# Optimization experiments

Hardware: AMD Instinct MI355X
Metric: run time of the kernel (lower is better)

Reference implementation:

```python
import jax, jax.numpy as jnp
import numpy as np

F = 256      # n_features
N = 128      # n_nodes
B = 4096     # batch


def setup_inputs() -> dict:
    key = jax.random.key(0)
    ks = jax.random.split(key, 11)
    s = lambda *sh: 1.0 / np.sqrt(sh[-2]) if len(sh) >= 2 else 1.0
    x = jax.random.normal(ks[0], (B, F), dtype=jnp.float32)
    # Block-diagonal weights: [F, in, out] per stage; biases [F, out]
    w1 = jax.random.normal(ks[1], (F, 1, N), dtype=jnp.float32)
    b1 = jax.random.normal(ks[2], (F, N), dtype=jnp.float32) * 0.01
    w2 = jax.random.normal(ks[3], (F, N, N), dtype=jnp.float32) / np.sqrt(N)
    b2 = jax.random.normal(ks[4], (F, N), dtype=jnp.float32) * 0.01
    w3 = jax.random.normal(ks[5], (F, N, N), dtype=jnp.float32) / np.sqrt(N)
    b3 = jax.random.normal(ks[6], (F, N), dtype=jnp.float32) * 0.01
    w4 = jax.random.normal(ks[7], (F, N, 1), dtype=jnp.float32) / np.sqrt(N)
    b4 = jax.random.normal(ks[8], (F, 1), dtype=jnp.float32) * 0.01
    # Final linear: [F, 1] weight, [1] bias
    lr_w = jax.random.normal(ks[9], (F, 1), dtype=jnp.float32) / np.sqrt(F)
    lr_b = jax.random.normal(ks[10], (1,), dtype=jnp.float32) * 0.01
    return {"x": x, "w1": w1, "b1": b1, "w2": w2, "b2": b2,
            "w3": w3, "b3": b3, "w4": w4, "b4": b4,
            "lr_w": lr_w, "lr_b": lr_b}


def reference(x, w1, b1, w2, b2, w3, b3, w4, b4, lr_w, lr_b):
    # Per-feature block-diagonal MLP chain with ReLU between stages.
    # x: [B, F] -> view each feature as a 1-dim input to its own subnet.
    h = x[:, :, None]                                   # [B, F, 1]
    h = jax.nn.relu(jnp.einsum('bfi,fio->bfo', h, w1) + b1)   # [B, F, N]
    h = jax.nn.relu(jnp.einsum('bfi,fio->bfo', h, w2) + b2)   # [B, F, N]
    h = jax.nn.relu(jnp.einsum('bfi,fio->bfo', h, w3) + b3)   # [B, F, N]
    h = jnp.einsum('bfi,fio->bfo', h, w4) + b4                # [B, F, 1]
    x_pre = h[:, :, 0]                                        # [B, F]
    return x_pre @ lr_w + lr_b                                # [B, 1]
```

## Files before the change

### kernel.cpp

```cpp
#include <hip/hip_runtime.h>
#include <hip/hip_bf16.h>

#define F_DIM 256
#define N_DIM 128
#define B_DIM 4096

typedef float f32x4v __attribute__((ext_vector_type(4)));
typedef float f32x16v __attribute__((ext_vector_type(16)));
typedef short s16x8 __attribute__((ext_vector_type(8)));
typedef unsigned int u32x4v __attribute__((ext_vector_type(4)));

#define PIN(x) asm("" : "+v"(x))

__device__ __forceinline__ unsigned short f2bf(float f) {
  union { float f; unsigned u; } v; v.f = f;
  unsigned r = v.u + 0x7fffu + ((v.u >> 16) & 1u);
  return (unsigned short)(r >> 16);
}

__device__ __forceinline__ unsigned pk2(float a, float b) {
  union { __hip_bfloat16 h[2]; unsigned u; } v;
  v.h[0] = __float2bfloat16(a);
  v.h[1] = __float2bfloat16(b);
  return v.u;
}

__device__ __forceinline__ void gload16(const void* g, void* l) {
  __builtin_amdgcn_global_load_lds(
      (const __attribute__((address_space(1))) unsigned int*)g,
      (__attribute__((address_space(3))) unsigned int*)l, 16, 0, 0);
}

__device__ __forceinline__ s16x8 frag1(unsigned d) {
  u32x4v v = {d, 0u, 0u, 0u};
  return __builtin_bit_cast(s16x8, v);
}

struct frag2 { s16x8 lo, hi; };

__device__ __forceinline__ frag2 cvt2(f32x16v a) {
  unsigned P[8];
#pragma unroll
  for (int q = 0; q < 8; ++q) {
    unsigned pk = pk2(a[2 * q], a[2 * q + 1]);
    asm("v_pk_max_i16 %0, %1, 0" : "=v"(P[q]) : "v"(pk));
  }
  u32x4v lo = {P[0], P[1], P[2], P[3]};
  u32x4v hh = {P[4], P[5], P[6], P[7]};
  frag2 r;
  r.lo = __builtin_bit_cast(s16x8, lo);
  r.hi = __builtin_bit_cast(s16x8, hh);
  return r;
}

__global__ void prep_w(const float* __restrict__ w2, const float* __restrict__ w3,
                       unsigned int* __restrict__ wTs) {
  __shared__ float tile[128 * 130];
  int m = blockIdx.x;
  const float* src = (m < 256) ? (w2 + (size_t)m * 16384)
                               : (w3 + (size_t)(m - 256) * 16384);
  int t = threadIdx.x;
  for (int k = 0; k < 64; ++k) {
    int idx = k * 256 + t;
    int i = idx >> 7, o = idx & 127;
    tile[o * 130 + i] = src[idx];
  }
  __syncthreads();
  unsigned int* dst = wTs + (size_t)m * 8192;
  for (int k = 0; k < 32; ++k) {
    int idx = k * 256 + t;
    int o = idx >> 6, i2 = idx & 63;
    unsigned pk = (unsigned)f2bf(tile[o * 130 + 2 * i2]) |
                  ((unsigned)f2bf(tile[o * 130 + 2 * i2 + 1]) << 16);
    int w = i2 & 7;
    int i2p = (i2 & ~7) + ((w >> 1) & 1) * 4 + (w & 1) + (((w >> 2) & 1) << 1);
    dst[(o * 64) + (i2p ^ ((o & 15) << 2))] = pk;
  }
}

__global__ void prep_x(const float* __restrict__ x, float* __restrict__ xT) {
  __shared__ float tile[64][65];
  int btile = blockIdx.x & 63;
  int ftile = blockIdx.x >> 6;
  int t = threadIdx.x;
  for (int k = 0; k < 16; ++k) {
    int idx = k * 256 + t;
    int r = idx >> 6, c = idx & 63;
    tile[r][c] = x[(size_t)(btile * 64 + r) * F_DIM + ftile * 64 + c];
  }
  __syncthreads();
  for (int k = 0; k < 16; ++k) {
    int idx = k * 256 + t;
    int fr = idx >> 6, br = idx & 63;
    xT[(size_t)(ftile * 64 + fr) * B_DIM + btile * 64 + br] = tile[br][fr];
  }
}

__global__ __launch_bounds__(256, 2) void mlp_chain(
    const float* __restrict__ xT, const float* __restrict__ w1,
    const float* __restrict__ b1, const float* __restrict__ b2,
    const float* __restrict__ b3, const float* __restrict__ w4,
    const float* __restrict__ b4, const unsigned int* __restrict__ wTs,
    float* __restrict__ xp) {
  __shared__ __align__(16) char Wb[2][128 * 256];
  __shared__ __align__(16) float w4l[N_DIM];

  const int f  = blockIdx.x >> 2;
  const int qt = blockIdx.x & 3;
  const int t  = threadIdx.x;
  const int lane = t & 63, wid = t >> 6;
  const int c32 = lane & 31, hi = lane >> 5;

  {
    const char* s2 = (const char*)(wTs + (size_t)f * 8192);
    const char* s3 = (const char*)(wTs + (size_t)(256 + f) * 8192);
#pragma unroll
    for (int c = 0; c < 8; ++c) {
      int off = (wid * 8 + c) * 1024;
      gload16(s2 + off + lane * 16, &Wb[0][off]);
    }
#pragma unroll
    for (int c = 0; c < 8; ++c) {
      int off = (wid * 8 + c) * 1024;
      gload16(s3 + off + lane * 16, &Wb[1][off]);
    }
    if (t < 32) *(f32x4v*)&w4l[t * 4] = *(const f32x4v*)&w4[f * N_DIM + t * 4];
  }

  unsigned a1d[4], a2d[4], a3d[4];
#pragma unroll
  for (int it = 0; it < 4; ++it) {
    int i = it * 32 + c32;
    float w1v = w1[f * N_DIM + i], b1v = b1[f * N_DIM + i];
    float b2v = b2[f * N_DIM + i], b3v = b3[f * N_DIM + i];
    a1d[it] = hi ? 0u : pk2(w1v, b1v);
    a2d[it] = hi ? 0u : pk2(0.f, b2v);
    a3d[it] = hi ? 0u : pk2(0.f, b3v);
  }
  const float b4f = b4[f];
  const float* xcol = xT + (size_t)f * B_DIM + qt * 1024;
  float* xprow = xp + (size_t)f * B_DIM + qt * 1024;

  const int wbase = c32 * 256 + (((lane & 15) ^ hi) << 4);
  int va[8];
#pragma unroll
  for (int m = 0; m < 8; ++m) { va[m] = wbase ^ (m << 5); PIN(va[m]); }
  const char* wb = &Wb[0][0];

  __syncthreads();

  const f32x16v zero = {0.f, 0.f, 0.f, 0.f, 0.f, 0.f, 0.f, 0.f,
                        0.f, 0.f, 0.f, 0.f, 0.f, 0.f, 0.f, 0.f};

  float xvA = xcol[wid * 64 + c32];
  float xvB = xcol[wid * 64 + 32 + c32];
#pragma unroll 1
  for (int itb = 0; itb < 4; ++itb) {
    const int bb = itb * 256 + wid * 64;
    s16x8 BxA = frag1(hi ? 0u : pk2(xvA, 1.0f));
    s16x8 BxB = frag1(hi ? 0u : pk2(xvB, 1.0f));
    float xvA_n = (itb < 3) ? xcol[bb + 256 + c32] : 0.f;
    float xvB_n = (itb < 3) ? xcol[bb + 256 + 32 + c32] : 0.f;

    s16x8 h1A[8], h1B[8];
#pragma unroll
    for (int it = 0; it < 4; ++it) {
      f32x16v hA = __builtin_amdgcn_mfma_f32_32x32x16_bf16(frag1(a1d[it]), BxA,
                                                           zero, 0, 0, 0);
      frag2 rA = cvt2(hA);
      h1A[2 * it] = rA.lo;  h1A[2 * it + 1] = rA.hi;
      PIN(h1A[2 * it]);  PIN(h1A[2 * it + 1]);
      f32x16v hB = __builtin_amdgcn_mfma_f32_32x32x16_bf16(frag1(a1d[it]), BxB,
                                                           zero, 0, 0, 0);
      frag2 rB = cvt2(hB);
      h1B[2 * it] = rB.lo;  h1B[2 * it + 1] = rB.hi;
      PIN(h1B[2 * it]);  PIN(h1B[2 * it + 1]);
    }

    s16x8 h2A[8], h2B[8];
#pragma unroll
    for (int ntp = 0; ntp < 2; ++ntp) {
      const int nt0 = 2 * ntp, nt1 = nt0 + 1;
      f32x16v u0A = __builtin_amdgcn_mfma_f32_32x32x16_bf16(frag1(a2d[nt0]), BxA,
                                                            zero, 0, 0, 0);
      f32x16v u0B = __builtin_amdgcn_mfma_f32_32x32x16_bf16(frag1(a2d[nt0]), BxB,
                                                            zero, 0, 0, 0);
      f32x16v u1A = __builtin_amdgcn_mfma_f32_32x32x16_bf16(frag1(a2d[nt1]), BxA,
                                                            zero, 0, 0, 0);
      f32x16v u1B = __builtin_amdgcn_mfma_f32_32x32x16_bf16(frag1(a2d[nt1]), BxB,
                                                            zero, 0, 0, 0);
      __builtin_amdgcn_s_setprio(1);
#pragma unroll
      for (int m = 0; m < 8; ++m) {
        s16x8 af0 = *(const s16x8*)(wb + va[m] + nt0 * 8192);
        s16x8 af1 = *(const s16x8*)(wb + va[m] + nt1 * 8192);
        u0A = __builtin_amdgcn_mfma_f32_32x32x16_bf16(af0, h1A[m], u0A, 0, 0, 0);
        u0B = __builtin_amdgcn_mfma_f32_32x32x16_bf16(af0, h1B[m], u0B, 0, 0, 0);
        u1A = __builtin_amdgcn_mfma_f32_32x32x16_bf16(af1, h1A[m], u1A, 0, 0, 0);
        u1B = __builtin_amdgcn_mfma_f32_32x32x16_bf16(af1, h1B[m], u1B, 0, 0, 0);
      }
      __builtin_amdgcn_s_setprio(0);
      frag2 r0A = cvt2(u0A);
      h2A[2 * nt0] = r0A.lo;  h2A[2 * nt0 + 1] = r0A.hi;
      PIN(h2A[2 * nt0]);  PIN(h2A[2 * nt0 + 1]);
      frag2 r0B = cvt2(u0B);
      h2B[2 * nt0] = r0B.lo;  h2B[2 * nt0 + 1] = r0B.hi;
      PIN(h2B[2 * nt0]);  PIN(h2B[2 * nt0 + 1]);
      frag2 r1A = cvt2(u1A);
      h2A[2 * nt1] = r1A.lo;  h2A[2 * nt1 + 1] = r1A.hi;
      PIN(h2A[2 * nt1]);  PIN(h2A[2 * nt1 + 1]);
      frag2 r1B = cvt2(u1B);
      h2B[2 * nt1] = r1B.lo;  h2B[2 * nt1 + 1] = r1B.hi;
      PIN(h2B[2 * nt1]);  PIN(h2B[2 * nt1 + 1]);
    }

    float pA = 0.f, pB = 0.f;
#pragma unroll
    for (int n3p = 0; n3p < 2; ++n3p) {
      const int n30 = 2 * n3p, n31 = n30 + 1;
      f32x16v v0A = __builtin_amdgcn_mfma_f32_32x32x16_bf16(frag1(a3d[n30]), BxA,
                                                            zero, 0, 0, 0);
      f32x16v v0B = __builtin_amdgcn_mfma_f32_32x32x16_bf16(frag1(a3d[n30]), BxB,
                                                            zero, 0, 0, 0);
      f32x16v v1A = __builtin_amdgcn_mfma_f32_32x32x16_bf16(frag1(a3d[n31]), BxA,
                                                            zero, 0, 0, 0);
      f32x16v v1B = __builtin_amdgcn_mfma_f32_32x32x16_bf16(frag1(a3d[n31]), BxB,
                                                            zero, 0, 0, 0);
      __builtin_amdgcn_s_setprio(1);
#pragma unroll
      for (int k = 0; k < 8; ++k) {
        s16x8 af0 = *(const s16x8*)(wb + va[k] + 32768 + n30 * 8192);
        s16x8 af1 = *(const s16x8*)(wb + va[k] + 32768 + n31 * 8192);
        v0A = __builtin_amdgcn_mfma_f32_32x32x16_bf16(af0, h2A[k], v0A, 0, 0, 0);
        v0B = __builtin_amdgcn_mfma_f32_32x32x16_bf16(af0, h2B[k], v0B, 0, 0, 0);
        v1A = __builtin_amdgcn_mfma_f32_32x32x16_bf16(af1, h2A[k], v1A, 0, 0, 0);
        v1B = __builtin_amdgcn_mfma_f32_32x32x16_bf16(af1, h2B[k], v1B, 0, 0, 0);
      }
      __builtin_amdgcn_s_setprio(0);
#pragma unroll
      for (int q = 0; q < 4; ++q) {
        f32x4v wv0 = *(const f32x4v*)&w4l[n30 * 32 + q * 8 + hi * 4];
        f32x4v wv1 = *(const f32x4v*)&w4l[n31 * 32 + q * 8 + hi * 4];
#pragma unroll
        for (int i = 0; i < 4; ++i) {
          pA = fmaf(fmaxf(v0A[4 * q + i], 0.f), wv0[i], pA);
          pB = fmaf(fmaxf(v0B[4 * q + i], 0.f), wv0[i], pB);
          pA = fmaf(fmaxf(v1A[4 * q + i], 0.f), wv1[i], pA);
          pB = fmaf(fmaxf(v1B[4 * q + i], 0.f), wv1[i], pB);
        }
      }
    }
    pA += __shfl_xor(pA, 32, 64);
    pB += __shfl_xor(pB, 32, 64);
    if (hi == 0) {
      xprow[bb + c32]      = pA + b4f;
      xprow[bb + 32 + c32] = pB + b4f;
    }
    xvA = xvA_n;
    xvB = xvB_n;
  }
}

__global__ void final_reduce(const float* __restrict__ xp,
                             const float* __restrict__ lr_w,
                             const float* __restrict__ lr_b,
                             float* __restrict__ out) {
  __shared__ float lw[F_DIM];
  __shared__ float part[4][64];
  int t = threadIdx.x;
  if (t < F_DIM) lw[t] = lr_w[t];
  __syncthreads();
  int q = t >> 6, bl = t & 63;
  int b = blockIdx.x * 64 + bl;
  float acc = 0.f;
#pragma unroll 8
  for (int j = 0; j < 64; ++j) {
    int ff = q * 64 + j;
    acc += xp[(size_t)ff * B_DIM + b] * lw[ff];
  }
  part[q][bl] = acc;
  __syncthreads();
  if (q == 0)
    out[b] = part[0][bl] + part[1][bl] + part[2][bl] + part[3][bl] + lr_b[0];
}

extern "C" void kernel_launch(void* const* d_in, const int* in_sizes, int n_in,
                              void* d_out, int out_size, void* d_ws, size_t ws_size,
                              hipStream_t stream) {
  (void)in_sizes; (void)n_in; (void)out_size; (void)ws_size;
  const float* x    = (const float*)d_in[0];
  const float* w1   = (const float*)d_in[1];
  const float* b1   = (const float*)d_in[2];
  const float* w2   = (const float*)d_in[3];
  const float* b2   = (const float*)d_in[4];
  const float* w3   = (const float*)d_in[5];
  const float* b3   = (const float*)d_in[6];
  const float* w4   = (const float*)d_in[7];
  const float* b4   = (const float*)d_in[8];
  const float* lr_w = (const float*)d_in[9];
  const float* lr_b = (const float*)d_in[10];
  float* out = (float*)d_out;

  char* ws = (char*)d_ws;
  unsigned int* wTs = (unsigned int*)ws;
  float* xT = (float*)(ws + (16u << 20));
  float* xp = (float*)(ws + (16u << 20) + (4u << 20));

  prep_w<<<512, 256, 0, stream>>>(w2, w3, wTs);
  prep_x<<<256, 256, 0, stream>>>(x, xT);
  mlp_chain<<<1024, 256, 0, stream>>>(xT, w1, b1, b2, b3, w4, b4, wTs, xp);
  final_reduce<<<64, 256, 0, stream>>>(xp, lr_w, lr_b, out);
}
```

Measured before the change: 97.51 us.

## Use 512-thread blocks per half-batch, reuse bias MFMAs, pack final dot as vec2

Result: slower. 201.4 us (+106.6%).

```diff
diff --git a/kernel.cpp b/kernel.cpp
--- a/kernel.cpp
+++ b/kernel.cpp
@@ -5,6 +5,7 @@
 #define N_DIM 128
 #define B_DIM 4096
 
+typedef float f32x2v __attribute__((ext_vector_type(2)));
 typedef float f32x4v __attribute__((ext_vector_type(4)));
 typedef float f32x16v __attribute__((ext_vector_type(16)));
 typedef short s16x8 __attribute__((ext_vector_type(8)));
@@ -96,7 +97,7 @@
   }
 }
 
-__global__ __launch_bounds__(256, 2) void mlp_chain(
+__global__ __launch_bounds__(512, 4) void mlp_chain(
     const float* __restrict__ xT, const float* __restrict__ w1,
     const float* __restrict__ b1, const float* __restrict__ b2,
     const float* __restrict__ b3, const float* __restrict__ w4,
@@ -105,9 +106,9 @@
   __shared__ __align__(16) char Wb[2][128 * 256];
   __shared__ __align__(16) float w4l[N_DIM];
 
-  const int f  = blockIdx.x >> 2;
-  const int qt = blockIdx.x & 3;
-  const int t  = threadIdx.x;
+  const int f    = blockIdx.x >> 1;
+  const int half = blockIdx.x & 1;
+  const int t    = threadIdx.x;
   const int lane = t & 63, wid = t >> 6;
   const int c32 = lane & 31, hi = lane >> 5;
 
@@ -115,13 +116,13 @@
     const char* s2 = (const char*)(wTs + (size_t)f * 8192);
     const char* s3 = (const char*)(wTs + (size_t)(256 + f) * 8192);
 #pragma unroll
-    for (int c = 0; c < 8; ++c) {
-      int off = (wid * 8 + c) * 1024;
+    for (int c = 0; c < 4; ++c) {
+      int off = (wid * 4 + c) * 1024;
       gload16(s2 + off + lane * 16, &Wb[0][off]);
     }
 #pragma unroll
-    for (int c = 0; c < 8; ++c) {
-      int off = (wid * 8 + c) * 1024;
+    for (int c = 0; c < 4; ++c) {
+      int off = (wid * 4 + c) * 1024;
       gload16(s3 + off + lane * 16, &Wb[1][off]);
     }
     if (t < 32) *(f32x4v*)&w4l[t * 4] = *(const f32x4v*)&w4[f * N_DIM + t * 4];
@@ -138,8 +139,8 @@
     a3d[it] = hi ? 0u : pk2(0.f, b3v);
   }
   const float b4f = b4[f];
-  const float* xcol = xT + (size_t)f * B_DIM + qt * 1024;
-  float* xprow = xp + (size_t)f * B_DIM + qt * 1024;
+  const float* xcol = xT + (size_t)f * B_DIM + half * 2048;
+  float* xprow = xp + (size_t)f * B_DIM + half * 2048;
 
   const int wbase = c32 * 256 + (((lane & 15) ^ hi) << 4);
   int va[8];
@@ -151,16 +152,17 @@
 
   const f32x16v zero = {0.f, 0.f, 0.f, 0.f, 0.f, 0.f, 0.f, 0.f,
                         0.f, 0.f, 0.f, 0.f, 0.f, 0.f, 0.f, 0.f};
+  const f32x2v zz = {0.f, 0.f};
 
   float xvA = xcol[wid * 64 + c32];
   float xvB = xcol[wid * 64 + 32 + c32];
 #pragma unroll 1
   for (int itb = 0; itb < 4; ++itb) {
-    const int bb = itb * 256 + wid * 64;
+    const int bb = itb * 512 + wid * 64;
     s16x8 BxA = frag1(hi ? 0u : pk2(xvA, 1.0f));
     s16x8 BxB = frag1(hi ? 0u : pk2(xvB, 1.0f));
-    float xvA_n = (itb < 3) ? xcol[bb + 256 + c32] : 0.f;
-    float xvB_n = (itb < 3) ? xcol[bb + 256 + 32 + c32] : 0.f;
+    float xvA_n = (itb < 3) ? xcol[bb + 512 + c32] : 0.f;
+    float xvB_n = (itb < 3) ? xcol[bb + 512 + 32 + c32] : 0.f;
 
     s16x8 h1A[8], h1B[8];
 #pragma unroll
@@ -181,23 +183,24 @@
 #pragma unroll
     for (int ntp = 0; ntp < 2; ++ntp) {
       const int nt0 = 2 * ntp, nt1 = nt0 + 1;
-      f32x16v u0A = __builtin_amdgcn_mfma_f32_32x32x16_bf16(frag1(a2d[nt0]), BxA,
+      f32x16v bi0 = __builtin_amdgcn_mfma_f32_32x32x16_bf16(frag1(a2d[nt0]), BxA,
                                                             zero, 0, 0, 0);
-      f32x16v u0B = __builtin_amdgcn_mfma_f32_32x32x16_bf16(frag1(a2d[nt0]), BxB,
+      f32x16v bi1 = __builtin_amdgcn_mfma_f32_32x32x16_bf16(frag1(a2d[nt1]), BxA,
                                                             zero, 0, 0, 0);
-      f32x16v u1A = __builtin_amdgcn_mfma_f32_32x32x16_bf16(frag1(a2d[nt1]), BxA,
-                                                            zero, 0, 0, 0);
-      f32x16v u1B = __builtin_amdgcn_mfma_f32_32x32x16_bf16(frag1(a2d[nt1]), BxB,
-                                                            zero, 0, 0, 0);
+      f32x16v u0A, u0B, u1A, u1B;
       __builtin_amdgcn_s_setprio(1);
 #pragma unroll
       for (int m = 0; m < 8; ++m) {
         s16x8 af0 = *(const s16x8*)(wb + va[m] + nt0 * 8192);
         s16x8 af1 = *(const s16x8*)(wb + va[m] + nt1 * 8192);
-        u0A = __builtin_amdgcn_mfma_f32_32x32x16_bf16(af0, h1A[m], u0A, 0, 0, 0);
-        u0B = __builtin_amdgcn_mfma_f32_32x32x16_bf16(af0, h1B[m], u0B, 0, 0, 0);
-        u1A = __builtin_amdgcn_mfma_f32_32x32x16_bf16(af1, h1A[m], u1A, 0, 0, 0);
-        u1B = __builtin_amdgcn_mfma_f32_32x32x16_bf16(af1, h1B[m], u1B, 0, 0, 0);
+        u0A = __builtin_amdgcn_mfma_f32_32x32x16_bf16(af0, h1A[m],
+                                                      m == 0 ? bi0 : u0A, 0, 0, 0);
+        u0B = __builtin_amdgcn_mfma_f32_32x32x16_bf16(af0, h1B[m],
+                                                      m == 0 ? bi0 : u0B, 0, 0, 0);
+        u1A = __builtin_amdgcn_mfma_f32_32x32x16_bf16(af1, h1A[m],
+                                                      m == 0 ? bi1 : u1A, 0, 0, 0);
+        u1B = __builtin_amdgcn_mfma_f32_32x32x16_bf16(af1, h1B[m],
+                                                      m == 0 ? bi1 : u1B, 0, 0, 0);
       }
       __builtin_amdgcn_s_setprio(0);
       frag2 r0A = cvt2(u0A);
@@ -214,42 +217,57 @@
       PIN(h2B[2 * nt1]);  PIN(h2B[2 * nt1 + 1]);
     }
 
-    float pA = 0.f, pB = 0.f;
+    f32x2v pA0 = zz, pA1 = zz, pB0 = zz, pB1 = zz;
 #pragma unroll
     for (int n3p = 0; n3p < 2; ++n3p) {
       const int n30 = 2 * n3p, n31 = n30 + 1;
-      f32x16v v0A = __builtin_amdgcn_mfma_f32_32x32x16_bf16(frag1(a3d[n30]), BxA,
+      f32x16v ci0 = __builtin_amdgcn_mfma_f32_32x32x16_bf16(frag1(a3d[n30]), BxA,
                                                             zero, 0, 0, 0);
-      f32x16v v0B = __builtin_amdgcn_mfma_f32_32x32x16_bf16(frag1(a3d[n30]), BxB,
+      f32x16v ci1 = __builtin_amdgcn_mfma_f32_32x32x16_bf16(frag1(a3d[n31]), BxA,
                                                             zero, 0, 0, 0);
-      f32x16v v1A = __builtin_amdgcn_mfma_f32_32x32x16_bf16(frag1(a3d[n31]), BxA,
-                                                            zero, 0, 0, 0);
-      f32x16v v1B = __builtin_amdgcn_mfma_f32_32x32x16_bf16(frag1(a3d[n31]), BxB,
-                                                            zero, 0, 0, 0);
+      f32x16v v0A, v0B, v1A, v1B;
       __builtin_amdgcn_s_setprio(1);
 #pragma unroll
       for (int k = 0; k < 8; ++k) {
         s16x8 af0 = *(const s16x8*)(wb + va[k] + 32768 + n30 * 8192);
         s16x8 af1 = *(const s16x8*)(wb + va[k] + 32768 + n31 * 8192);
-        v0A = __builtin_amdgcn_mfma_f32_32x32x16_bf16(af0, h2A[k], v0A, 0, 0, 0);
-        v0B = __builtin_amdgcn_mfma_f32_32x32x16_bf16(af0, h2B[k], v0B, 0, 0, 0);
-        v1A = __builtin_amdgcn_mfma_f32_32x32x16_bf16(af1, h2A[k], v1A, 0, 0, 0);
-        v1B = __builtin_amdgcn_mfma_f32_32x32x16_bf16(af1, h2B[k], v1B, 0, 0, 0);
+        v0A = __builtin_amdgcn_mfma_f32_32x32x16_bf16(af0, h2A[k],
+                                                      k == 0 ? ci0 : v0A, 0, 0, 0);
+        v0B = __builtin_amdgcn_mfma_f32_32x32x16_bf16(af0, h2B[k],
+                                                      k == 0 ? ci0 : v0B, 0, 0, 0);
+        v1A = __builtin_amdgcn_mfma_f32_32x32x16_bf16(af1, h2A[k],
+                                                      k == 0 ? ci1 : v1A, 0, 0, 0);
+        v1B = __builtin_amdgcn_mfma_f32_32x32x16_bf16(af1, h2B[k],
+                                                      k == 0 ? ci1 : v1B, 0, 0, 0);
       }
       __builtin_amdgcn_s_setprio(0);
 #pragma unroll
       for (int q = 0; q < 4; ++q) {
-        f32x4v wv0 = *(const f32x4v*)&w4l[n30 * 32 + q * 8 + hi * 4];
-        f32x4v wv1 = *(const f32x4v*)&w4l[n31 * 32 + q * 8 + hi * 4];
-#pragma unroll
-        for (int i = 0; i < 4; ++i) {
-          pA = fmaf(fmaxf(v0A[4 * q + i], 0.f), wv0[i], pA);
-          pB = fmaf(fmaxf(v0B[4 * q + i], 0.f), wv0[i], pB);
-          pA = fmaf(fmaxf(v1A[4 * q + i], 0.f), wv1[i], pA);
-          pB = fmaf(fmaxf(v1B[4 * q + i], 0.f), wv1[i], pB);
-        }
+        f32x2v w01_0 = *(const f32x2v*)&w4l[n30 * 32 + q * 8 + hi * 4];
+        f32x2v w23_0 = *(const f32x2v*)&w4l[n30 * 32 + q * 8 + hi * 4 + 2];
+        f32x2v w01_1 = *(const f32x2v*)&w4l[n31 * 32 + q * 8 + hi * 4];
+        f32x2v w23_1 = *(const f32x2v*)&w4l[n31 * 32 + q * 8 + hi * 4 + 2];
+        f32x2v r;
+        r[0] = fmaxf(v0A[4 * q + 0], 0.f); r[1] = fmaxf(v0A[4 * q + 1], 0.f);
+        pA0 += r * w01_0;
+        r[0] = fmaxf(v0A[4 * q + 2], 0.f); r[1] = fmaxf(v0A[4 * q + 3], 0.f);
+        pA1 += r * w23_0;
+        r[0] = fmaxf(v1A[4 * q + 0], 0.f); r[1] = fmaxf(v1A[4 * q + 1], 0.f);
+        pA0 += r * w01_1;
+        r[0] = fmaxf(v1A[4 * q + 2], 0.f); r[1] = fmaxf(v1A[4 * q + 3], 0.f);
+        pA1 += r * w23_1;
+        r[0] = fmaxf(v0B[4 * q + 0], 0.f); r[1] = fmaxf(v0B[4 * q + 1], 0.f);
+        pB0 += r * w01_0;
+        r[0] = fmaxf(v0B[4 * q + 2], 0.f); r[1] = fmaxf(v0B[4 * q + 3], 0.f);
+        pB1 += r * w23_0;
+        r[0] = fmaxf(v1B[4 * q + 0], 0.f); r[1] = fmaxf(v1B[4 * q + 1], 0.f);
+        pB0 += r * w01_1;
+        r[0] = fmaxf(v1B[4 * q + 2], 0.f); r[1] = fmaxf(v1B[4 * q + 3], 0.f);
+        pB1 += r * w23_1;
       }
     }
+    float pA = pA0[0] + pA0[1] + pA1[0] + pA1[1];
+    float pB = pB0[0] + pB0[1] + pB1[0] + pB1[1];
     pA += __shfl_xor(pA, 32, 64);
     pB += __shfl_xor(pB, 32, 64);
     if (hi == 0) {
@@ -308,6 +326,6 @@
 
   prep_w<<<512, 256, 0, stream>>>(w2, w3, wTs);
   prep_x<<<256, 256, 0, stream>>>(x, xT);
-  mlp_chain<<<1024, 256, 0, stream>>>(xT, w1, b1, b2, b3, w4, b4, wTs, xp);
+  mlp_chain<<<512, 512, 0, stream>>>(xT, w1, b1, b2, b3, w4, b4, wTs, xp);
   final_reduce<<<64, 256, 0, stream>>>(xp, lr_w, lr_b, out);
 }
```
